# Performance work log

Hardware: AMD Instinct MI355X
Metric: run time of the kernel (lower is better)

The kernel has to match this reference:

```python
import jax, jax.numpy as jnp
import numpy as np

N_NODES = 50000
N_EDGES = 1000000
IN_F = 128
OUT_F = 128
K = 4
NEG_SLOPE = 0.01  # torch nn.LeakyReLU() default
EPS = 1e-8


def setup_inputs() -> dict:
    key = jax.random.key(0)
    k1, k2, k3, k4, k5, k6 = jax.random.split(key, 6)
    x = jax.random.normal(k1, (N_NODES, IN_F), dtype=jnp.float32)
    e = jax.random.uniform(k2, (N_NODES, K), dtype=jnp.float32)
    stdv = 1.0 / np.sqrt(OUT_F)
    weights = jax.random.uniform(k3, (K, IN_F, OUT_F), minval=-stdv, maxval=stdv, dtype=jnp.float32)
    a = jax.random.normal(k4, (K, 2 * OUT_F, 1), dtype=jnp.float32) * 0.1
    # edge_index with no self-loops (remove_self_loops is then a no-op)
    row = jax.random.randint(k5, (N_EDGES,), 0, N_NODES)
    off = jax.random.randint(k6, (N_EDGES,), 1, N_NODES)
    col = (row + off) % N_NODES
    adj = jnp.stack([row, col]).astype(jnp.int64)
    return {"x": x, "e": e, "weights": weights, "a": a, "adj": adj}


def _canet_gat_forward(x, e, weights, a, adj):
    N = x.shape[0]
    out_f = weights.shape[-1]
    # add self loops (input has none)
    loops = jnp.arange(N, dtype=adj.dtype)
    src = jnp.concatenate([adj[0], loops])  # [Et]
    dst = jnp.concatenate([adj[1], loops])  # [Et]

    # per-head projection: [K, N, O]
    h = jnp.einsum('nd,kdo->kno', x, weights)

    # attention logits: a = [a_src; a_dst], logit_e = leakyrelu(h[src].a_src + h[dst].a_dst)
    a_src = a[:, :out_f, 0]   # [K, O]
    a_dst = a[:, out_f:, 0]   # [K, O]
    s_src = jnp.einsum('kno,ko->kn', h, a_src)  # [K, N]
    s_dst = jnp.einsum('kno,ko->kn', h, a_dst)  # [K, N]
    logits = s_src[:, src] + s_dst[:, dst]      # [K, Et]
    logits = jnp.where(logits >= 0, logits, NEG_SLOPE * logits)
    logits_max = jnp.max(logits, axis=1, keepdims=True)  # global max per head
    edge_e = jnp.exp(logits - logits_max)                # [K, Et]

    outputs = []
    for k in range(h.shape[0]):  # small fixed loop over heads (avoids [K,Et,O] blowup)
        denom = jax.ops.segment_sum(edge_e[k], src, num_segments=N) + EPS   # [N]
        msg = edge_e[k][:, None] * h[k][dst]                                # [Et, O]
        hi_k = jax.ops.segment_sum(msg, src, num_segments=N)                # [N, O]
        outputs.append(hi_k / denom[:, None])
    outputs = jnp.stack(outputs, axis=1)  # [N, K, O]

    out = jnp.sum(e[:, :, None] * outputs, axis=1)  # [N, O]
    return out + x  # residual (in_features == out_features)


def reference(x, e, weights, a, adj):
    return _canet_gat_forward(x, e, weights, a, adj)
```

## Files before the change

kernel.cpp:

```cpp
#include <hip/hip_runtime.h>
#include <hip/hip_bf16.h>
#include <cstddef>

#define NN 50000
#define NE 1000000
#define F  128
#define KH 4
#define NEG 0.01f
#define EPSF 1e-8f
#define CAP 64
#define NBIN 196
#define BINCAP 8192
#define EPB 16384
#define NB1 ((NE + EPB - 1) / EPB)
#define NBW 256
#define NBP 2048
#define STR (NBP * 4)
#define MXSTR 32
#define TSTR 32

typedef short bf16x8 __attribute__((ext_vector_type(8)));
typedef float f32x4 __attribute__((ext_vector_type(4)));

__device__ inline ushort f2bf(float f) {
    __hip_bfloat16 b = __float2bfloat16(f);
    return *reinterpret_cast<ushort*>(&b);
}
__device__ inline unsigned int packbf(float xl, float xh) {
    return (unsigned int)f2bf(xl) | ((unsigned int)f2bf(xh) << 16);
}
__device__ inline float lk(float v) { return (v >= 0.f) ? v : NEG * v; }

__global__ __launch_bounds__(256) void bin_kernel(const int* __restrict__ adj,
                                                  int* __restrict__ binTail,
                                                  unsigned int* __restrict__ binbuf,
                                                  const float* __restrict__ W,
                                                  const float* __restrict__ a,
                                                  ushort* __restrict__ wt,
                                                  float* __restrict__ vvg) {
    int b = blockIdx.x;
    int tid = threadIdx.x;
    if (b < NB1) {
        __shared__ int hist[NBIN];
        int base = b * EPB;
        int nloc = min(EPB, NE - base);
        for (int i = tid; i < NBIN; i += 256) hist[i] = 0;
        __syncthreads();
        for (int off = tid; off < nloc; off += 256) {
            unsigned int s = (unsigned int)adj[base + off];
            atomicAdd(&hist[s >> 8], 1);
        }
        __syncthreads();
        for (int i = tid; i < NBIN; i += 256) {
            int c = hist[i];
            hist[i] = atomicAdd(&binTail[i * TSTR], c);
        }
        __syncthreads();
        for (int off = tid; off < nloc; off += 256) {
            int e = base + off;
            unsigned int s = (unsigned int)adj[e];
            unsigned int d = (unsigned int)adj[NE + e];
            int bn = s >> 8;
            int p = atomicAdd(&hist[bn], 1);
            if (p < BINCAP) binbuf[(size_t)bn * BINCAP + p] = (s << 16) | d;
        }
    } else if (b < NB1 + NBW) {
        int i = (b - NB1) * 256 + tid;
        int k = i >> 14;
        int dd = (i >> 7) & 127;
        int o = i & 127;
        wt[((size_t)k * F + o) * F + dd] = f2bf(W[i]);
    } else {
        int j0 = tid * 4;
#pragma unroll
        for (int ii = 0; ii < 4; ii++) {
            int j = j0 + ii;
            int side = j >> 9;
            int k = (j >> 7) & 3;
            int dd = j & 127;
            const float4* Wr = (const float4*)(W + (size_t)k * F * F + (size_t)dd * F);
            const float4* ar = (const float4*)(a + (size_t)k * 2 * F + side * F);
            float acc = 0.f;
#pragma unroll 8
            for (int o = 0; o < F / 4; o++) {
                float4 wv = Wr[o], av = ar[o];
                acc += wv.x * av.x + wv.y * av.y + wv.z * av.z + wv.w * av.w;
            }
            vvg[j] = acc;
        }
    }
}

__global__ __launch_bounds__(256) void build_prep_kernel(const int* __restrict__ binTail,
                                                         const unsigned int* __restrict__ binbuf,
                                                         int* __restrict__ cnt,
                                                         ushort* __restrict__ bucket16,
                                                         const float* __restrict__ vvg,
                                                         const float* __restrict__ x,
                                                         unsigned int* __restrict__ xb2,
                                                         float* __restrict__ ssrc4,
                                                         float* __restrict__ sdst4,
                                                         int* __restrict__ mxsi) {
    int tid = threadIdx.x;
    __shared__ __align__(16) int shmem[1024];
    __shared__ float bmax_s[4][8];

    if (blockIdx.x < NBIN) {
        int b = blockIdx.x;
        int* lcnt = shmem;
        int* lpos = shmem + 256;
        lcnt[tid] = 0;
        lpos[tid] = 0;
        __syncthreads();
        int tail = min(binTail[b * TSTR], BINCAP);
        const unsigned int* bb = binbuf + (size_t)b * BINCAP;
        for (int i = tid; i < tail; i += 256) {
            unsigned int pk = bb[i];
            atomicAdd(&lcnt[(pk >> 16) & 255], 1);
        }
        __syncthreads();
        int n0 = b << 8;
        cnt[n0 + tid] = lcnt[tid];
        for (int i = tid; i < tail; i += 256) {
            unsigned int pk = bb[i];
            int sl = (pk >> 16) & 255;
            int p = atomicAdd(&lpos[sl], 1);
            if (p < CAP) bucket16[(size_t)(n0 + sl) * CAP + p] = (ushort)(pk & 0xffffu);
        }
        return;
    }

    float* vvf = (float*)shmem;
    ((float4*)vvf)[tid] = ((const float4*)vvg)[tid];
    __syncthreads();

    int wv = tid >> 6, lane = tid & 63;
    int gw = (blockIdx.x - NBIN) * 4 + wv;
    const float2* x2 = (const float2*)x;
    float2 vs[4], vd[4];
#pragma unroll
    for (int k = 0; k < 4; k++) {
        vs[k] = *(const float2*)&vvf[k * F + 2 * lane];
        vd[k] = *(const float2*)&vvf[(4 + k) * F + 2 * lane];
    }
    int l1 = lane & 1, l2 = lane & 2, l4 = lane & 4;
    int j = 4 * l1 + l2 + (l4 >> 2);
    float* sp = (j < 4) ? (ssrc4 + j) : (sdst4 + (j - 4));
    float mxv = 0.f;

    for (int n = gw; n < NN; n += 2 * STR) {
        int nb = n + STR;
        bool vb = nb < NN;
        float2 xa = x2[(size_t)n * 64 + lane];
        float2 xbv = vb ? x2[(size_t)nb * 64 + lane] : make_float2(0.f, 0.f);
        xb2[(size_t)n * 64 + lane] = packbf(xa.x, xa.y);
        if (vb) xb2[(size_t)nb * 64 + lane] = packbf(xbv.x, xbv.y);
        float s[8], q[8];
#pragma unroll
        for (int k = 0; k < 4; k++) {
            s[k]     = xa.x * vs[k].x + xa.y * vs[k].y;
            s[4 + k] = xa.x * vd[k].x + xa.y * vd[k].y;
            q[k]     = xbv.x * vs[k].x + xbv.y * vs[k].y;
            q[4 + k] = xbv.x * vd[k].x + xbv.y * vd[k].y;
        }
        float tA[4], tB[4];
#pragma unroll
        for (int i = 0; i < 4; i++) {
            float mA = l1 ? s[4 + i] : s[i];
            float oA = __shfl_xor(l1 ? s[i] : s[4 + i], 1);
            tA[i] = mA + oA;
            float mB = l1 ? q[4 + i] : q[i];
            float oB = __shfl_xor(l1 ? q[i] : q[4 + i], 1);
            tB[i] = mB + oB;
        }
        float uA[2], uB[2];
#pragma unroll
        for (int i = 0; i < 2; i++) {
            float mA = l2 ? tA[2 + i] : tA[i];
            float oA = __shfl_xor(l2 ? tA[i] : tA[2 + i], 2);
            uA[i] = mA + oA;
            float mB = l2 ? tB[2 + i] : tB[i];
            float oB = __shfl_xor(l2 ? tB[i] : tB[2 + i], 2);
            uB[i] = mB + oB;
        }
        float vA, vB;
        {
            float mA = l4 ? uA[1] : uA[0];
            float oA = __shfl_xor(l4 ? uA[0] : uA[1], 4);
            vA = mA + oA;
            float mB = l4 ? uB[1] : uB[0];
            float oB = __shfl_xor(l4 ? uB[0] : uB[1], 4);
            vB = mB + oB;
        }
        vA += __shfl_xor(vA, 8);  vB += __shfl_xor(vB, 8);
        vA += __shfl_xor(vA, 16); vB += __shfl_xor(vB, 16);
        vA += __shfl_xor(vA, 32); vB += __shfl_xor(vB, 32);
        if (lane < 8) {
            sp[(size_t)n * 4] = vA;
            if (vb) sp[(size_t)nb * 4] = vB;
        }
        mxv = fmaxf(mxv, fmaxf(vA, vB));
    }
    if (lane < 8) bmax_s[wv][j] = mxv;
    __syncthreads();
    if (tid < 8) {
        float m = fmaxf(fmaxf(bmax_s[0][tid], bmax_s[1][tid]),
                        fmaxf(bmax_s[2][tid], bmax_s[3][tid]));
        atomicMax(&mxsi[tid * MXSTR], __float_as_int(m));
    }
}

__global__ __launch_bounds__(256) void aggregate_kernel(const unsigned int* __restrict__ xb2,
                                                        const float* __restrict__ ssrc4,
                                                        const float* __restrict__ sdst4,
                                                        const float* __restrict__ mxs,
                                                        const int* __restrict__ cnt,
                                                        const ushort* __restrict__ bucket16,
                                                        const float* __restrict__ ew,
                                                        unsigned int* __restrict__ z2) {
    int wv = threadIdx.x >> 6, lane = threadIdx.x & 63;
    int n = blockIdx.x * 4 + wv;
    if (n >= NN) return;

    __shared__ int dsh[4][64];
    __shared__ __align__(16) float wsh[4][64][4];

    float m0 = lk(mxs[0 * MXSTR] + mxs[4 * MXSTR]);
    float m1 = lk(mxs[1 * MXSTR] + mxs[5 * MXSTR]);
    float m2 = lk(mxs[2 * MXSTR] + mxs[6 * MXSTR]);
    float m3 = lk(mxs[3 * MXSTR] + mxs[7 * MXSTR]);
    float4 ss  = *(const float4*)&ssrc4[(size_t)n * 4];
    float4 sdn = *(const float4*)&sdst4[(size_t)n * 4];
    float w0s = __expf(lk(ss.x + sdn.x) - m0);
    float w1s = __expf(lk(ss.y + sdn.y) - m1);
    float w2s = __expf(lk(ss.z + sdn.z) - m2);
    float w3s = __expf(lk(ss.w + sdn.w) - m3);

    int deg = min(cnt[n], CAP);
    float4 w = make_float4(0.f, 0.f, 0.f, 0.f);
    int d = 0;
    if (lane < deg) {
        d = (int)bucket16[(size_t)n * CAP + lane];
        float4 sd = *(const float4*)&sdst4[(size_t)d * 4];
        w.x = __expf(lk(ss.x + sd.x) - m0);
        w.y = __expf(lk(ss.y + sd.y) - m1);
        w.z = __expf(lk(ss.z + sd.z) - m2);
        w.w = __expf(lk(ss.w + sd.w) - m3);
    }
    dsh[wv][lane] = d;
    *(float4*)&wsh[wv][lane][0] = w;

    float dn0 = w.x, dn1 = w.y, dn2 = w.z, dn3 = w.w;
#pragma unroll
    for (int st = 1; st < 64; st <<= 1) {
        dn0 += __shfl_xor(dn0, st);
        dn1 += __shfl_xor(dn1, st);
        dn2 += __shfl_xor(dn2, st);
        dn3 += __shfl_xor(dn3, st);
    }

    float a0[4], a1[4];
    {
        unsigned int v = xb2[(size_t)n * 64 + lane];
        union { unsigned int u; float f; } lo, hi;
        lo.u = v << 16;
        hi.u = v & 0xffff0000u;
        a0[0] = w0s * lo.f; a1[0] = w0s * hi.f;
        a0[1] = w1s * lo.f; a1[1] = w1s * hi.f;
        a0[2] = w2s * lo.f; a1[2] = w2s * hi.f;
        a0[3] = w3s * lo.f; a1[3] = w3s * hi.f;
    }

    int degp = (deg + 7) & ~7;
    for (int i = 0; i < degp; i += 8) {
        int du[8];
#pragma unroll
        for (int u = 0; u < 8; u++)
            du[u] = __builtin_amdgcn_readfirstlane(dsh[wv][i + u]);
        unsigned int vu[8];
#pragma unroll
        for (int u = 0; u < 8; u++)
            vu[u] = xb2[(size_t)du[u] * 64 + lane];
#pragma unroll
        for (int u = 0; u < 8; u++) {
            float4 w4 = *(const float4*)&wsh[wv][i + u][0];
            union { unsigned int uu; float f; } lo, hi;
            lo.uu = vu[u] << 16;
            hi.uu = vu[u] & 0xffff0000u;
            a0[0] += w4.x * lo.f; a1[0] += w4.x * hi.f;
            a0[1] += w4.y * lo.f; a1[1] += w4.y * hi.f;
            a0[2] += w4.z * lo.f; a1[2] += w4.z * hi.f;
            a0[3] += w4.w * lo.f; a1[3] += w4.w * hi.f;
        }
    }

    float4 e4 = *(const float4*)&ew[(size_t)n * 4];
    float i0 = e4.x / (w0s + dn0 + EPSF);
    float i1 = e4.y / (w1s + dn1 + EPSF);
    float i2 = e4.z / (w2s + dn2 + EPSF);
    float i3 = e4.w / (w3s + dn3 + EPSF);
    size_t zb = (size_t)n * 256;
    z2[zb +   0 + lane] = packbf(a0[0] * i0, a1[0] * i0);
    z2[zb +  64 + lane] = packbf(a0[1] * i1, a1[1] * i1);
    z2[zb + 128 + lane] = packbf(a0[2] * i2, a1[2] * i2);
    z2[zb + 192 + lane] = packbf(a0[3] * i3, a1[3] * i3);
}

#define MT 64
__global__ __launch_bounds__(256) void gemm2_kernel(const ushort* __restrict__ z,
                                                    const ushort* __restrict__ wt,
                                                    const float* __restrict__ x,
                                                    float* __restrict__ out) {
    int row0 = blockIdx.x * MT;
    int tid = threadIdx.x;
    int wave = tid >> 6, lane = tid & 63;
    int quad = lane >> 4, l16 = lane & 15;
    __shared__ ushort ws[F][136];

    int arow = row0 + wave * 16 + l16;
    if (arow >= NN) arow = NN - 1;

    f32x4 acc[8];
#pragma unroll
    for (int i = 0; i < 8; i++) acc[i] = (f32x4){0.f, 0.f, 0.f, 0.f};

    for (int k = 0; k < KH; k++) {
        __syncthreads();
        const ushort* wk = wt + (size_t)k * F * F;
        for (int i = tid; i < F * 16; i += 256) {
            int r = i >> 4, c = (i & 15) * 8;
            *(uint4*)&ws[r][c] = *(const uint4*)&wk[r * F + c];
        }
        __syncthreads();
#pragma unroll
        for (int kt = 0; kt < 4; kt++) {
            int kb = kt * 32 + quad * 8;
            bf16x8 af = *(const bf16x8*)&z[(size_t)arow * 512 + k * F + kb];
#pragma unroll
            for (int ni = 0; ni < 8; ni++) {
                bf16x8 bf = *(const bf16x8*)&ws[ni * 16 + l16][kb];
                acc[ni] = __builtin_amdgcn_mfma_f32_16x16x32_bf16(af, bf, acc[ni], 0, 0, 0);
            }
        }
    }
#pragma unroll
    for (int r = 0; r < 4; r++) {
        int n = row0 + wave * 16 + quad * 4 + r;
        if (n < NN) {
#pragma unroll
            for (int ni = 0; ni < 8; ni++) {
                int o = ni * 16 + l16;
                out[(size_t)n * F + o] = x[(size_t)n * F + o] + acc[ni][r];
            }
        }
    }
}

extern "C" void kernel_launch(void* const* d_in, const int* in_sizes, int n_in,
                              void* d_out, int out_size, void* d_ws, size_t ws_size,
                              hipStream_t stream) {
    const float* x = (const float*)d_in[0];
    const float* e = (const float*)d_in[1];
    const float* W = (const float*)d_in[2];
    const float* a = (const float*)d_in[3];
    const int*   adj = (const int*)d_in[4];
    float* out = (float*)d_out;

    char* ws = (char*)d_ws;
    auto take = [&](size_t bytes) {
        char* p = ws;
        ws += (bytes + 255) & ~(size_t)255;
        return p;
    };
    ushort* z      = (ushort*)take((size_t)NN * KH * F * sizeof(ushort));
    unsigned int* xb2 = (unsigned int*)take((size_t)NN * F * sizeof(ushort));
    ushort* wt     = (ushort*)take((size_t)KH * F * F * sizeof(ushort));
    float* ssrc4   = (float*)take((size_t)NN * 4 * sizeof(float));
    float* sdst4   = (float*)take((size_t)NN * 4 * sizeof(float));
    int*   cnt     = (int*)take((size_t)NBIN * 256 * sizeof(int));
    ushort* bucket16 = (ushort*)take((size_t)NBIN * 256 * CAP * sizeof(ushort));
    unsigned int* binbuf = (unsigned int*)take((size_t)NBIN * BINCAP * sizeof(unsigned int));
    int*   binTail = (int*)take((size_t)NBIN * TSTR * sizeof(int));
    float* mxs     = (float*)take((size_t)8 * MXSTR * sizeof(float));
    float* vvg     = (float*)take((size_t)8 * F * sizeof(float));

    hipMemsetAsync(binTail, 0, (size_t)NBIN * TSTR * sizeof(int), stream);
    hipMemsetAsync(mxs, 0, (size_t)8 * MXSTR * sizeof(float), stream);
    bin_kernel<<<NB1 + NBW + 1, 256, 0, stream>>>(adj, binTail, binbuf, W, a, wt, vvg);
    build_prep_kernel<<<NBIN + NBP, 256, 0, stream>>>(binTail, binbuf, cnt, bucket16,
                                                      vvg, x, xb2, ssrc4, sdst4, (int*)mxs);
    aggregate_kernel<<<(NN + 3) / 4, 256, 0, stream>>>(xb2, ssrc4, sdst4, mxs, cnt,
                                                       bucket16, e, (unsigned int*)z);
    gemm2_kernel<<<(NN + MT - 1) / MT, 256, 0, stream>>>(z, wt, x, out);
}
```

Before: 243.2 us.

## Split edge binning across sub-blocks per chunk and deepen gather unroll to 16

Each edge chunk in the binning kernel is now handled by four blocks, each owning the bins whose index matches its sub-id modulo four. Adjacency loads are batched eight per thread to raise memory-level parallelism, and fewer LDS atomics land in each block. The cost is that every sub-block re-reads the whole chunk of src/dst indices. Separately, the neighbor gather loop is unrolled 16 deep instead of 8 to keep more loads in flight, at the price of more padding work for low-degree nodes, which relies on the dsh/wsh padding covering 16 entries.

```diff
diff --git a/kernel.cpp b/kernel.cpp
--- a/kernel.cpp
+++ b/kernel.cpp
@@ -12,7 +12,9 @@
 #define NBIN 196
 #define BINCAP 8192
 #define EPB 16384
-#define NB1 ((NE + EPB - 1) / EPB)
+#define SUBS 4
+#define NCH ((NE + EPB - 1) / EPB)
+#define NB1 (NCH * SUBS)
 #define NBW 256
 #define NBP 2048
 #define STR (NBP * 4)
@@ -42,27 +44,52 @@
     int tid = threadIdx.x;
     if (b < NB1) {
         __shared__ int hist[NBIN];
-        int base = b * EPB;
+        int chunk = b >> 2, sub = b & (SUBS - 1);
+        int base = chunk * EPB;
         int nloc = min(EPB, NE - base);
         for (int i = tid; i < NBIN; i += 256) hist[i] = 0;
         __syncthreads();
-        for (int off = tid; off < nloc; off += 256) {
-            unsigned int s = (unsigned int)adj[base + off];
-            atomicAdd(&hist[s >> 8], 1);
+        for (int off0 = 0; off0 < EPB; off0 += 256 * 8) {
+            int sv[8]; bool va[8];
+#pragma unroll
+            for (int u = 0; u < 8; u++) {
+                int off = off0 + u * 256 + tid;
+                va[u] = off < nloc;
+                sv[u] = adj[base + (va[u] ? off : 0)];
+            }
+#pragma unroll
+            for (int u = 0; u < 8; u++) {
+                int bn = ((unsigned int)sv[u]) >> 8;
+                if (va[u] && (bn & (SUBS - 1)) == sub) atomicAdd(&hist[bn], 1);
+            }
         }
         __syncthreads();
         for (int i = tid; i < NBIN; i += 256) {
-            int c = hist[i];
-            hist[i] = atomicAdd(&binTail[i * TSTR], c);
-        }
-        __syncthreads();
-        for (int off = tid; off < nloc; off += 256) {
-            int e = base + off;
-            unsigned int s = (unsigned int)adj[e];
-            unsigned int d = (unsigned int)adj[NE + e];
-            int bn = s >> 8;
-            int p = atomicAdd(&hist[bn], 1);
-            if (p < BINCAP) binbuf[(size_t)bn * BINCAP + p] = (s << 16) | d;
+            if ((i & (SUBS - 1)) == sub) {
+                int c = hist[i];
+                hist[i] = atomicAdd(&binTail[i * TSTR], c);
+            }
+        }
+        __syncthreads();
+        for (int off0 = 0; off0 < EPB; off0 += 256 * 8) {
+            int sv[8], dv[8]; bool va[8];
+#pragma unroll
+            for (int u = 0; u < 8; u++) {
+                int off = off0 + u * 256 + tid;
+                va[u] = off < nloc;
+                int e = base + (va[u] ? off : 0);
+                sv[u] = adj[e];
+                dv[u] = adj[NE + e];
+            }
+#pragma unroll
+            for (int u = 0; u < 8; u++) {
+                unsigned int s = (unsigned int)sv[u];
+                int bn = s >> 8;
+                if (va[u] && (bn & (SUBS - 1)) == sub) {
+                    int p = atomicAdd(&hist[bn], 1);
+                    if (p < BINCAP) binbuf[(size_t)bn * BINCAP + p] = (s << 16) | (unsigned int)dv[u];
+                }
+            }
         }
     } else if (b < NB1 + NBW) {
         int i = (b - NB1) * 256 + tid;
@@ -271,18 +298,18 @@
         a0[3] = w3s * lo.f; a1[3] = w3s * hi.f;
     }
 
-    int degp = (deg + 7) & ~7;
-    for (int i = 0; i < degp; i += 8) {
-        int du[8];
-#pragma unroll
-        for (int u = 0; u < 8; u++)
+    int degp = (deg + 15) & ~15;
+    for (int i = 0; i < degp; i += 16) {
+        int du[16];
+#pragma unroll
+        for (int u = 0; u < 16; u++)
             du[u] = __builtin_amdgcn_readfirstlane(dsh[wv][i + u]);
-        unsigned int vu[8];
-#pragma unroll
-        for (int u = 0; u < 8; u++)
+        unsigned int vu[16];
+#pragma unroll
+        for (int u = 0; u < 16; u++)
             vu[u] = xb2[(size_t)du[u] * 64 + lane];
 #pragma unroll
-        for (int u = 0; u < 8; u++) {
+        for (int u = 0; u < 16; u++) {
             float4 w4 = *(const float4*)&wsh[wv][i + u][0];
             union { unsigned int uu; float f; } lo, hi;
             lo.uu = vu[u] << 16;
```

Measured after the change: 239.1 us. About the same (-1.7%).
